# Kernel optimization log

Measured on AMD Instinct MI355X. Metric: run time of the kernel, lower is better.

## Reference

```python
import jax, jax.numpy as jnp
import numpy as np

MIN_NORM = 1e-15
EPS = 1e-7
MASK_FILL = -9e15


def logmap0(x, c):
    # Hyperboloid log map at the origin (HGCN convention, K = 1/c)
    K = 1.0 / c
    sqrtK = K ** 0.5
    y = x[:, 1:]
    y_norm = jnp.clip(jnp.linalg.norm(y, axis=-1, keepdims=True), MIN_NORM)
    theta = jnp.clip(x[:, :1] / sqrtK, 1.0 + EPS)
    res = sqrtK * jnp.arccosh(theta) * y / y_norm
    return jnp.concatenate([jnp.zeros_like(x[:, :1]), res], axis=1)


def proj(x, c):
    # normalize: recompute time coordinate so x lies on the hyperboloid
    K = 1.0 / c
    y = x[:, 1:]
    x0 = jnp.sqrt(K + jnp.sum(y * y, axis=-1, keepdims=True))
    return jnp.concatenate([x0, y], axis=1)


def expmap0(u, c):
    K = 1.0 / c
    sqrtK = K ** 0.5
    x = u[:, 1:]
    x_norm = jnp.clip(jnp.linalg.norm(x, axis=-1, keepdims=True), MIN_NORM)
    theta = x_norm / sqrtK
    res = jnp.concatenate(
        [sqrtK * jnp.cosh(theta), sqrtK * jnp.sinh(theta) * x / x_norm], axis=1
    )
    return proj(res, c)


def setup_inputs() -> dict:
    key = jax.random.key(0)
    k1, k2, k3, k4, k5 = jax.random.split(key, 5)
    N, D_in, D_out = 8192, 256, 256
    x = jax.random.normal(k1, (N, D_in), dtype=jnp.float32)
    adj = jax.random.randint(k2, (N, N), 0, 2, dtype=jnp.int32)
    W_gcn = jax.random.normal(k3, (D_in - 1, D_out - 1), dtype=jnp.float32)
    # xavier_uniform-like scale (gain=1.414)
    std_w = 1.414 * (2.0 / (D_out + D_out)) ** 0.5
    W_att = jax.random.normal(k4, (D_out, D_out), dtype=jnp.float32) * std_w
    std_a = 1.414 * (2.0 / (2 * D_out + 1)) ** 0.5
    a_att = jax.random.normal(k5, (2 * D_out, 1), dtype=jnp.float32) * std_a
    return {"x": x, "adj": adj, "k": 1, "W_gcn": W_gcn, "W_att": W_att, "a_att": a_att}


def reference(x, adj, k, W_gcn, W_att, a_att):
    c = float(k)  # curvature
    N = x.shape[0]
    # tangent-space linear map, keeping time coordinate zero
    logx = logmap0(x, c)
    Wx = logx[:, 1:] @ W_gcn  # [N, D_out-1]
    tmp = jnp.concatenate([jnp.zeros((N, 1), x.dtype), Wx], axis=1)
    fun7 = proj(expmap0(tmp, c), c)  # expmap0 + normalize
    h_in = logmap0(fun7, c)  # [N, D_out]
    # GraphAttentionLayer (dense GAT; a_input @ a decomposes into rank-1 terms)
    h = h_in @ W_att  # [N, F]
    F_ = h.shape[1]
    e = (h @ a_att[:F_]) + (h @ a_att[F_:]).T  # [N, N]; == cat([h_i, h_j]) @ a
    att = jnp.where(adj > 0, e, MASK_FILL)
    att = jax.nn.softmax(att, axis=1)  # dropout omitted (eval mode)
    h_prime = att @ h
    emb = jax.nn.elu(h_prime)  # concat=True
    emb = proj(emb, c)  # manifold.normalize
    # HypAct with sigmoid
    out = expmap0(jax.nn.sigmoid(logmap0(emb, c)), c)
    return out
```

## Files before the change

### kernel.cpp

```cpp
#include <hip/hip_runtime.h>
#include <hip/hip_bf16.h>
#include <math.h>

typedef __attribute__((ext_vector_type(4))) float f32x4;
typedef __attribute__((ext_vector_type(8))) short bf16x8;

#define N_ROWS 8192
#define D 256
#define MSHIFT 16.0f
#define NKB 8
#define KRANGE (N_ROWS / NKB)
#define NSTEP (KRANGE / 32)

__device__ __forceinline__ unsigned short f2bf(float f) {
    unsigned int u = __float_as_uint(f);
    unsigned int r = u + 0x7FFFu + ((u >> 16) & 1u);
    return (unsigned short)(r >> 16);
}
__device__ __forceinline__ float bf2f(unsigned short h) {
    return __uint_as_float(((unsigned int)h) << 16);
}

__device__ __forceinline__ float breduce_sum256(float v, float* sb) {
#pragma unroll
    for (int off = 32; off; off >>= 1) v += __shfl_down(v, off);
    int wid = threadIdx.x >> 6;
    __syncthreads();
    if ((threadIdx.x & 63) == 0) sb[wid] = v;
    __syncthreads();
    return sb[0] + sb[1] + sb[2] + sb[3];
}

__device__ __forceinline__ void dma16(const void* g, void* l) {
    __builtin_amdgcn_global_load_lds(
        (const __attribute__((address_space(1))) unsigned int*)g,
        (__attribute__((address_space(3))) unsigned int*)l, 16, 0, 0);
}

__device__ __forceinline__ bf16x8 adj2bf(int4 a, int4 b) {
    bf16x8 r;
    r[0] = a.x ? (short)0x3F80 : (short)0;
    r[1] = a.y ? (short)0x3F80 : (short)0;
    r[2] = a.z ? (short)0x3F80 : (short)0;
    r[3] = a.w ? (short)0x3F80 : (short)0;
    r[4] = b.x ? (short)0x3F80 : (short)0;
    r[5] = b.y ? (short)0x3F80 : (short)0;
    r[6] = b.z ? (short)0x3F80 : (short)0;
    r[7] = b.w ? (short)0x3F80 : (short)0;
    return r;
}

__global__ void k_M2v(const float* __restrict__ Wg, const float* __restrict__ Wa,
                      const float* __restrict__ aatt,
                      unsigned short* __restrict__ M2Thi, unsigned short* __restrict__ M2Tlo,
                      float* __restrict__ v) {
    __shared__ float sb[4];
    int k = blockIdx.x, t = threadIdx.x;
    float acc = 0.f;
#pragma unroll 8
    for (int m = 0; m < 255; ++m)
        acc += Wg[k * 255 + m] * Wa[(m + 1) * 256 + t];
    unsigned short hi = f2bf(acc);
    unsigned short lo = f2bf(acc - bf2f(hi));
    M2Thi[t * 256 + k] = hi;
    M2Tlo[t * 256 + k] = lo;
    if (k == 0) { M2Thi[t * 256 + 255] = 0; M2Tlo[t * 256 + 255] = 0; }
    float s = breduce_sum256(acc * aatt[256 + t], sb);
    if (t == 0) v[k] = s;
}

__global__ void k_logw(const float* __restrict__ x, const float* __restrict__ v,
                       unsigned short* __restrict__ wbf,
                       unsigned short* __restrict__ Awhi, unsigned short* __restrict__ Awlo) {
    __shared__ float sb[4];
    int i0 = blockIdx.x * 8, t = threadIdx.x;
    float vv = (t >= 1) ? v[t - 1] : 0.f;
#pragma unroll
    for (int r = 0; r < 8; ++r) {
        float xv = x[(size_t)(i0 + r) * D + t];
        float yv = (t >= 1) ? xv : 0.f;
        float ss = breduce_sum256(yv * yv, sb);
        float x0 = x[(size_t)(i0 + r) * D];
        float coef = acoshf(fmaxf(x0, 1.f + 1e-7f)) / fmaxf(sqrtf(ss), 1e-15f);
        float lg = coef * yv;
        float c = breduce_sum256(lg * vv, sb);
        float w = expf(c - MSHIFT);
        if (t == r) wbf[i0 + r] = f2bf(w);
        float aw = w * lg;
        unsigned short hi = f2bf(aw);
        unsigned short lo = f2bf(aw - bf2f(hi));
        int kd = (t == 0) ? 255 : (t - 1);
        Awhi[(size_t)(i0 + r) * 256 + kd] = hi;
        Awlo[(size_t)(i0 + r) * 256 + kd] = lo;
    }
}

__global__ void __launch_bounds__(512)
k_hGT(const unsigned short* __restrict__ M2Thi, const unsigned short* __restrict__ M2Tlo,
      const unsigned short* __restrict__ Awhi, const unsigned short* __restrict__ Awlo,
      unsigned short* __restrict__ GT) {
    __shared__ __align__(16) char ahi[32768], alo[32768], bhi[8192], blo[8192];
    const int tid = threadIdx.x;
    const int w = tid >> 6, l = tid & 63;
    const int lr = l & 15, lq = l >> 4;
    const int i0 = blockIdx.x * 64;
    const int gs = (l & 7) ^ (l >> 3);

    const unsigned short* srcAhi[4];
    const unsigned short* srcAlo[4];
#pragma unroll
    for (int i = 0; i < 4; ++i) {
        int rowA = (w * 4 + i) * 8 + (l >> 3);
        srcAhi[i] = M2Thi + rowA * 256 + gs * 8;
        srcAlo[i] = M2Tlo + rowA * 256 + gs * 8;
    }
    int rowB = w * 8 + (l >> 3);
    const unsigned short* srcBhi = Awhi + (size_t)(i0 + rowB) * 256 + gs * 8;
    const unsigned short* srcBlo = Awlo + (size_t)(i0 + rowB) * 256 + gs * 8;

    f32x4 zero4 = {0.f, 0.f, 0.f, 0.f};
    f32x4 acc[2][4];
#pragma unroll
    for (int m = 0; m < 2; ++m)
#pragma unroll
        for (int n = 0; n < 4; ++n) acc[m][n] = zero4;

    for (int t = 0; t < 4; ++t) {
        if (t) __syncthreads();
#pragma unroll
        for (int i = 0; i < 4; ++i) {
            dma16(srcAhi[i] + t * 64, ahi + (w * 4 + i) * 1024);
            dma16(srcAlo[i] + t * 64, alo + (w * 4 + i) * 1024);
        }
        dma16(srcBhi + t * 64, bhi + w * 1024);
        dma16(srcBlo + t * 64, blo + w * 1024);
        asm volatile("s_waitcnt vmcnt(0)" ::: "memory");
        __syncthreads();
#pragma unroll
        for (int ks = 0; ks < 2; ++ks) {
            const int g = ((ks * 4 + lq) ^ (lr & 7)) * 16;
            bf16x8 afh[2], afl[2];
#pragma unroll
            for (int m = 0; m < 2; ++m) {
                int row = w * 32 + m * 16 + lr;
                afh[m] = *(const bf16x8*)(ahi + row * 128 + g);
                afl[m] = *(const bf16x8*)(alo + row * 128 + g);
            }
#pragma unroll
            for (int n = 0; n < 4; ++n) {
                int rb = n * 16 + lr;
                bf16x8 bfh = *(const bf16x8*)(bhi + rb * 128 + g);
                bf16x8 bfl = *(const bf16x8*)(blo + rb * 128 + g);
#pragma unroll
                for (int m = 0; m < 2; ++m) {
                    acc[m][n] = __builtin_amdgcn_mfma_f32_16x16x32_bf16(afh[m], bfh, acc[m][n], 0, 0, 0);
                    acc[m][n] = __builtin_amdgcn_mfma_f32_16x16x32_bf16(afh[m], bfl, acc[m][n], 0, 0, 0);
                    acc[m][n] = __builtin_amdgcn_mfma_f32_16x16x32_bf16(afl[m], bfh, acc[m][n], 0, 0, 0);
                }
            }
        }
    }
#pragma unroll
    for (int m = 0; m < 2; ++m)
#pragma unroll
        for (int n = 0; n < 4; ++n)
#pragma unroll
            for (int vv = 0; vv < 4; ++vv) {
                int c = w * 32 + m * 16 + lq * 4 + vv;
                GT[(size_t)c * N_ROWS + i0 + n * 16 + lr] = f2bf(acc[m][n][vv]);
            }
}

__global__ void __launch_bounds__(512, 2)
k_attadj(const int* __restrict__ adj, const unsigned short* __restrict__ GT,
         const unsigned short* __restrict__ wbf, unsigned short* __restrict__ part,
         float* __restrict__ rspart) {
    __shared__ __align__(16) char bufA[3 * 32768];
    __shared__ __align__(16) char bufB[3 * 16384];
    __shared__ __align__(16) char wlds[2048];
    const int tid = threadIdx.x;
    const int kb = blockIdx.x & 7;
    const int rb = blockIdx.x >> 3;
    const int i0 = rb * 256;
    const int kbeg = kb * KRANGE;
    const int w = tid >> 6, l = tid & 63;
    const int lr = l & 15, lq = l >> 4;
    const int wm = w >> 1, wn = w & 1;

    const int row8 = l >> 3, gA = (l & 7) ^ row8;
    const int* srcA[4];
#pragma unroll
    for (int i = 0; i < 4; ++i) {
        int a = w * 4 + i;
        srcA[i] = adj + (size_t)(i0 + a * 8 + row8) * N_ROWS + kbeg + gA * 4;
    }
    const int col4 = l >> 2, gB = ((l & 3) ^ (col4 & 3)) * 8;
    const unsigned short* srcB[2];
#pragma unroll
    for (int i = 0; i < 2; ++i) {
        int b = w * 2 + i;
        srcB[i] = GT + (size_t)(b * 16 + col4) * N_ROWS + kbeg + gB;
    }

#define STAGE(T_, BI_) do {                                                \
        _Pragma("unroll")                                                  \
        for (int i_ = 0; i_ < 4; ++i_)                                     \
            dma16(srcA[i_] + (T_) * 32, bufA + (BI_) * 32768 + (w * 4 + i_) * 1024); \
        _Pragma("unroll")                                                  \
        for (int i_ = 0; i_ < 2; ++i_)                                     \
            dma16(srcB[i_] + (T_) * 32, bufB + (BI_) * 16384 + (w * 2 + i_) * 1024); \
    } while (0)

    f32x4 zero4 = {0.f, 0.f, 0.f, 0.f};
    f32x4 acc[4][8], acc_rs[4];
#pragma unroll
    for (int m = 0; m < 4; ++m) {
        acc_rs[m] = zero4;
#pragma unroll
        for (int n = 0; n < 8; ++n) acc[m][n] = zero4;
    }

    STAGE(0, 0);
    if (w < 2) dma16(wbf + kbeg + w * 512 + l * 8, wlds + w * 1024);

    int cb = 0;
    for (int t = 0; t < NSTEP; ++t) {
        int nb = (cb == 2) ? 0 : cb + 1;
        if (t + 1 < NSTEP) {
            STAGE(t + 1, nb);
            asm volatile("s_waitcnt vmcnt(6)" ::: "memory");
        } else {
            asm volatile("s_waitcnt vmcnt(0)" ::: "memory");
        }
        __builtin_amdgcn_sched_barrier(0);
        __builtin_amdgcn_s_barrier();
        __builtin_amdgcn_sched_barrier(0);

        const char* bA = bufA + cb * 32768;
        const char* bB = bufB + cb * 16384;

        bf16x8 wf = {0, 0, 0, 0, 0, 0, 0, 0};
        if (lr == 0) wf = *(const bf16x8*)(wlds + t * 64 + lq * 16);

        bf16x8 af[4];
#pragma unroll
        for (int m = 0; m < 4; ++m) {
            int row = wm * 64 + m * 16 + lr;
            int4 u  = *(const int4*)(bA + row * 128 + (((2 * lq) ^ (lr & 7)) << 4));
            int4 v2 = *(const int4*)(bA + row * 128 + (((2 * lq + 1) ^ (lr & 7)) << 4));
            af[m] = adj2bf(u, v2);
            acc_rs[m] = __builtin_amdgcn_mfma_f32_16x16x32_bf16(af[m], wf, acc_rs[m], 0, 0, 0);
        }
#pragma unroll
        for (int n = 0; n < 8; ++n) {
            int col = wn * 128 + n * 16 + lr;
            bf16x8 bf = *(const bf16x8*)(bB + col * 64 + ((lq ^ (lr & 3)) << 4));
#pragma unroll
            for (int m = 0; m < 4; ++m)
                acc[m][n] = __builtin_amdgcn_mfma_f32_16x16x32_bf16(af[m], bf, acc[m][n], 0, 0, 0);
        }
        cb = nb;
    }
#undef STAGE

    if (wn == 0 && lr == 0) {
#pragma unroll
        for (int m = 0; m < 4; ++m)
#pragma unroll
            for (int vv = 0; vv < 4; ++vv)
                rspart[(size_t)kb * N_ROWS + i0 + wm * 64 + m * 16 + lq * 4 + vv] = acc_rs[m][vv];
    }

    unsigned short* pbase = part + (size_t)kb * N_ROWS * D;
#pragma unroll
    for (int m = 0; m < 4; ++m)
#pragma unroll
        for (int n = 0; n < 8; ++n) {
            int orow = i0 + wm * 64 + m * 16 + lq * 4;
            int ocol = wn * 128 + n * 16 + lr;
            unsigned short* op = pbase + (size_t)orow * D + ocol;
#pragma unroll
            for (int vv = 0; vv < 4; ++vv)
                __builtin_nontemporal_store(f2bf(acc[m][n][vv]), op + (size_t)vv * D);
        }
}

__global__ void k_final3(const unsigned short* __restrict__ part, const float* __restrict__ rspart,
                         float* __restrict__ out) {
    __shared__ float sb[4];
    int row = blockIdx.x, t = threadIdx.x;
    float raw = 0.f, rs = 0.f;
#pragma unroll
    for (int kbi = 0; kbi < NKB; ++kbi) {
        raw += bf2f(__builtin_nontemporal_load(&part[((size_t)kbi * N_ROWS + row) * D + t]));
        rs += rspart[(size_t)kbi * N_ROWS + row];
    }
    float hp = raw / rs;
    float ey = 0.f;
    if (t >= 1) ey = (hp > 0.f) ? hp : expm1f(hp);
    float ss = breduce_sum256(ey * ey, sb);
    float x0 = sqrtf(1.f + ss);
    float th = fmaxf(x0, 1.f + 1e-7f);
    float al = acoshf(th);
    float yn = fmaxf(sqrtf(ss), 1e-15f);
    float u = (t >= 1) ? (al * ey / yn) : 0.f;
    float s = 1.f / (1.f + expf(-u));
    float s2 = (t >= 1) ? s * s : 0.f;
    float ssn = breduce_sum256(s2, sb);
    float xn = fmaxf(sqrtf(ssn), 1e-15f);
    float sh = sinhf(xn);
    float yf = (t >= 1) ? (sh * s / xn) : 0.f;
    float sy = breduce_sum256(yf * yf, sb);
    float res = (t == 0) ? sqrtf(1.f + sy) : yf;
    out[(size_t)row * D + t] = res;
}

extern "C" void kernel_launch(void* const* d_in, const int* in_sizes, int n_in,
                              void* d_out, int out_size, void* d_ws, size_t ws_size,
                              hipStream_t stream) {
    const float* x    = (const float*)d_in[0];
    const int*   adj  = (const int*)d_in[1];
    const float* Wg   = (const float*)d_in[3];
    const float* Wa   = (const float*)d_in[4];
    const float* aatt = (const float*)d_in[5];
    float* out = (float*)d_out;

    char* wsb = (char*)d_ws;
    unsigned short* M2Thi  = (unsigned short*)(wsb);
    unsigned short* M2Tlo  = (unsigned short*)(wsb + 0x0020000);
    float*          v      = (float*)(wsb + 0x0040000);
    unsigned short* wbf    = (unsigned short*)(wsb + 0x0048000);
    unsigned short* Awhi   = (unsigned short*)(wsb + 0x0100000);
    unsigned short* Awlo   = (unsigned short*)(wsb + 0x0500000);
    unsigned short* GT     = (unsigned short*)(wsb + 0x0900000);
    float*          rspart = (float*)(wsb + 0x0D00000);
    unsigned short* part   = (unsigned short*)(wsb + 0x1000000);

    k_M2v<<<255, 256, 0, stream>>>(Wg, Wa, aatt, M2Thi, M2Tlo, v);
    k_logw<<<N_ROWS / 8, 256, 0, stream>>>(x, v, wbf, Awhi, Awlo);
    k_hGT<<<N_ROWS / 64, 512, 0, stream>>>(M2Thi, M2Tlo, Awhi, Awlo, GT);
    k_attadj<<<32 * NKB, 512, 0, stream>>>(adj, GT, wbf, part, rspart);
    k_final3<<<N_ROWS, 256, 0, stream>>>(part, rspart, out);
}
```

Baseline: 155.3 us.

## Use one wavefront per row in logw and halve the row tile in hGT

k_logw now assigns one 64-lane wavefront per row. Each lane handles 4 contiguous columns, reductions use shuffles, and stores are vectorized 4-wide, replacing two block-wide LDS reductions per row with sequential rows per block. The column permutation changes so that v[255]=0 covers the time coordinate, with index 255 written in k_M2v. k_hGT processes 32 rows per block instead of 64, doubling the grid to 256 blocks for better CU occupancy, at the cost of reloading the M2T tiles twice as often per row.

```diff
diff --git a/kernel.cpp b/kernel.cpp
--- a/kernel.cpp
+++ b/kernel.cpp
@@ -4,6 +4,7 @@
 
 typedef __attribute__((ext_vector_type(4))) float f32x4;
 typedef __attribute__((ext_vector_type(8))) short bf16x8;
+typedef __attribute__((ext_vector_type(4))) unsigned short u16x4;
 
 #define N_ROWS 8192
 #define D 256
@@ -66,44 +67,58 @@
     M2Tlo[t * 256 + k] = lo;
     if (k == 0) { M2Thi[t * 256 + 255] = 0; M2Tlo[t * 256 + 255] = 0; }
     float s = breduce_sum256(acc * aatt[256 + t], sb);
-    if (t == 0) v[k] = s;
-}
-
-__global__ void k_logw(const float* __restrict__ x, const float* __restrict__ v,
-                       unsigned short* __restrict__ wbf,
-                       unsigned short* __restrict__ Awhi, unsigned short* __restrict__ Awlo) {
-    __shared__ float sb[4];
-    int i0 = blockIdx.x * 8, t = threadIdx.x;
-    float vv = (t >= 1) ? v[t - 1] : 0.f;
-#pragma unroll
-    for (int r = 0; r < 8; ++r) {
-        float xv = x[(size_t)(i0 + r) * D + t];
-        float yv = (t >= 1) ? xv : 0.f;
-        float ss = breduce_sum256(yv * yv, sb);
-        float x0 = x[(size_t)(i0 + r) * D];
-        float coef = acoshf(fmaxf(x0, 1.f + 1e-7f)) / fmaxf(sqrtf(ss), 1e-15f);
-        float lg = coef * yv;
-        float c = breduce_sum256(lg * vv, sb);
-        float w = expf(c - MSHIFT);
-        if (t == r) wbf[i0 + r] = f2bf(w);
-        float aw = w * lg;
+    if (t == 0) { v[k] = s; if (k == 0) v[255] = 0.f; }
+}
+
+__global__ void __launch_bounds__(512)
+k_logw(const float* __restrict__ x, const float* __restrict__ v,
+       unsigned short* __restrict__ wbf,
+       unsigned short* __restrict__ Awhi, unsigned short* __restrict__ Awlo) {
+    const int tid = threadIdx.x;
+    const int w = tid >> 6, l = tid & 63;
+    const int row = blockIdx.x * 8 + w;
+    const float* xr = x + (size_t)row * D;
+    float xv[4];
+#pragma unroll
+    for (int j = 0; j < 4; ++j) {
+        int c = l * 4 + 1 + j;
+        xv[j] = (c < 256) ? xr[c] : 0.f;
+    }
+    float ss = xv[0] * xv[0] + xv[1] * xv[1] + xv[2] * xv[2] + xv[3] * xv[3];
+#pragma unroll
+    for (int off = 32; off; off >>= 1) ss += __shfl_xor(ss, off);
+    float x0 = xr[0];
+    float coef = acoshf(fmaxf(x0, 1.f + 1e-7f)) / fmaxf(sqrtf(ss), 1e-15f);
+    float lg[4];
+#pragma unroll
+    for (int j = 0; j < 4; ++j) lg[j] = coef * xv[j];
+    float4 vv = *(const float4*)(v + l * 4);
+    float cdot = lg[0] * vv.x + lg[1] * vv.y + lg[2] * vv.z + lg[3] * vv.w;
+#pragma unroll
+    for (int off = 32; off; off >>= 1) cdot += __shfl_xor(cdot, off);
+    float wv = expf(cdot - MSHIFT);
+    if (l == 0) wbf[row] = f2bf(wv);
+    u16x4 hi4, lo4;
+#pragma unroll
+    for (int j = 0; j < 4; ++j) {
+        float aw = wv * lg[j];
         unsigned short hi = f2bf(aw);
-        unsigned short lo = f2bf(aw - bf2f(hi));
-        int kd = (t == 0) ? 255 : (t - 1);
-        Awhi[(size_t)(i0 + r) * 256 + kd] = hi;
-        Awlo[(size_t)(i0 + r) * 256 + kd] = lo;
-    }
+        hi4[j] = hi;
+        lo4[j] = f2bf(aw - bf2f(hi));
+    }
+    *(u16x4*)(Awhi + (size_t)row * 256 + l * 4) = hi4;
+    *(u16x4*)(Awlo + (size_t)row * 256 + l * 4) = lo4;
 }
 
 __global__ void __launch_bounds__(512)
 k_hGT(const unsigned short* __restrict__ M2Thi, const unsigned short* __restrict__ M2Tlo,
       const unsigned short* __restrict__ Awhi, const unsigned short* __restrict__ Awlo,
       unsigned short* __restrict__ GT) {
-    __shared__ __align__(16) char ahi[32768], alo[32768], bhi[8192], blo[8192];
+    __shared__ __align__(16) char ahi[32768], alo[32768], bhi[4096], blo[4096];
     const int tid = threadIdx.x;
     const int w = tid >> 6, l = tid & 63;
     const int lr = l & 15, lq = l >> 4;
-    const int i0 = blockIdx.x * 64;
+    const int i0 = blockIdx.x * 32;
     const int gs = (l & 7) ^ (l >> 3);
 
     const unsigned short* srcAhi[4];
@@ -114,16 +129,17 @@
         srcAhi[i] = M2Thi + rowA * 256 + gs * 8;
         srcAlo[i] = M2Tlo + rowA * 256 + gs * 8;
     }
-    int rowB = w * 8 + (l >> 3);
-    const unsigned short* srcBhi = Awhi + (size_t)(i0 + rowB) * 256 + gs * 8;
-    const unsigned short* srcBlo = Awlo + (size_t)(i0 + rowB) * 256 + gs * 8;
+    const int jb = w & 3;
+    const int rowB = jb * 8 + (l >> 3);
+    const unsigned short* srcB = ((w < 4) ? Awhi : Awlo) + (size_t)(i0 + rowB) * 256 + gs * 8;
+    char* dstB = ((w < 4) ? bhi : blo) + jb * 1024;
 
     f32x4 zero4 = {0.f, 0.f, 0.f, 0.f};
-    f32x4 acc[2][4];
+    f32x4 acc[2][2];
 #pragma unroll
     for (int m = 0; m < 2; ++m)
 #pragma unroll
-        for (int n = 0; n < 4; ++n) acc[m][n] = zero4;
+        for (int n = 0; n < 2; ++n) acc[m][n] = zero4;
 
     for (int t = 0; t < 4; ++t) {
         if (t) __syncthreads();
@@ -132,8 +148,7 @@
             dma16(srcAhi[i] + t * 64, ahi + (w * 4 + i) * 1024);
             dma16(srcAlo[i] + t * 64, alo + (w * 4 + i) * 1024);
         }
-        dma16(srcBhi + t * 64, bhi + w * 1024);
-        dma16(srcBlo + t * 64, blo + w * 1024);
+        dma16(srcB + t * 64, dstB);
         asm volatile("s_waitcnt vmcnt(0)" ::: "memory");
         __syncthreads();
 #pragma unroll
@@ -147,7 +162,7 @@
                 afl[m] = *(const bf16x8*)(alo + row * 128 + g);
             }
 #pragma unroll
-            for (int n = 0; n < 4; ++n) {
+            for (int n = 0; n < 2; ++n) {
                 int rb = n * 16 + lr;
                 bf16x8 bfh = *(const bf16x8*)(bhi + rb * 128 + g);
                 bf16x8 bfl = *(const bf16x8*)(blo + rb * 128 + g);
@@ -163,7 +178,7 @@
 #pragma unroll
     for (int m = 0; m < 2; ++m)
 #pragma unroll
-        for (int n = 0; n < 4; ++n)
+        for (int n = 0; n < 2; ++n)
 #pragma unroll
             for (int vv = 0; vv < 4; ++vv) {
                 int c = w * 32 + m * 16 + lq * 4 + vv;
@@ -337,8 +352,8 @@
     unsigned short* part   = (unsigned short*)(wsb + 0x1000000);
 
     k_M2v<<<255, 256, 0, stream>>>(Wg, Wa, aatt, M2Thi, M2Tlo, v);
-    k_logw<<<N_ROWS / 8, 256, 0, stream>>>(x, v, wbf, Awhi, Awlo);
-    k_hGT<<<N_ROWS / 64, 512, 0, stream>>>(M2Thi, M2Tlo, Awhi, Awlo, GT);
+    k_logw<<<N_ROWS / 8, 512, 0, stream>>>(x, v, wbf, Awhi, Awlo);
+    k_hGT<<<N_ROWS / 32, 512, 0, stream>>>(M2Thi, M2Tlo, Awhi, Awlo, GT);
     k_attadj<<<32 * NKB, 512, 0, stream>>>(adj, GT, wbf, part, rspart);
     k_final3<<<N_ROWS, 256, 0, stream>>>(part, rspart, out);
 }
```

After: 147.4 us (median of 2 runs). -5.1%, faster.
